# Performance work log

Measured on AMD Instinct MI355X. Metric: run time of the kernel, lower is better.

## Reference

```python
import jax, jax.numpy as jnp
import numpy as np
from jax import lax

THR = 1.0
SLOPE = 25.0
EPS = 1e-5

@jax.custom_vjp
def spike(u):
    # Heaviside with fast-sigmoid surrogate gradient (slope=25)
    return (u > 0.0).astype(u.dtype)

def _spike_fwd(u):
    return (u > 0.0).astype(u.dtype), u

def _spike_bwd(u, g):
    return (g / (SLOPE * jnp.abs(u) + 1.0) ** 2,)

spike.defvjp(_spike_fwd, _spike_bwd)

def lif_scan(inp, beta):
    # inp: (T, B, H); snntorch Leaky, reset_mechanism='subtract', init mem=0
    def step(mem, cur):
        reset = lax.stop_gradient(spike(mem - THR))
        mem = beta * mem + cur - reset * THR
        spk = spike(mem - THR)
        return mem, (spk, mem)
    mem0 = jnp.zeros(inp.shape[1:], inp.dtype)
    _, (spk, mem) = lax.scan(step, mem0, inp)
    return spk, mem

def bn_per_step(h, g, b):
    # h: (T, B, H); training-mode BatchNorm1d applied per timestep over batch
    m = h.mean(axis=1, keepdims=True)
    v = h.var(axis=1, keepdims=True)
    return (h - m) / jnp.sqrt(v + EPS) * g + b

def setup_inputs() -> dict:
    key = jax.random.key(0)
    ks = jax.random.split(key, 16)
    B, T, C = 128, 128, 32
    H, Ts, HOR, K = 512, 4, 96, 3
    s = 0.02
    return {
        "x": jax.random.normal(ks[0], (B, T, C), jnp.float32),
        "conv_w": jax.random.normal(ks[1], (H * Ts, C, K), jnp.float32) * s,
        "conv_b": jnp.zeros((H * Ts,), jnp.float32),
        "bn1_g": jnp.ones((H * Ts,), jnp.float32),
        "bn1_b": jnp.zeros((H * Ts,), jnp.float32),
        "beta_enc": jnp.full((H,), 0.9, jnp.float32),
        "bn2_g": jnp.ones((H,), jnp.float32),
        "bn2_b": jnp.zeros((H,), jnp.float32),
        "beta2": jnp.full((H,), 0.9, jnp.float32),
        "bn3_g": jnp.ones((H,), jnp.float32),
        "bn3_b": jnp.zeros((H,), jnp.float32),
        "beta3": jnp.full((H,), 0.9, jnp.float32),
        "wq": jax.random.normal(ks[2], (H, H), jnp.float32) * s,
        "bq": jnp.zeros((H,), jnp.float32),
        "wk": jax.random.normal(ks[3], (H, H), jnp.float32) * s,
        "bk": jnp.zeros((H,), jnp.float32),
        "wv": jax.random.normal(ks[4], (H, H), jnp.float32) * s,
        "bv": jnp.zeros((H,), jnp.float32),
        "bna_g": jnp.ones((H,), jnp.float32),
        "bna_b": jnp.zeros((H,), jnp.float32),
        "wh": jax.random.normal(ks[5], (HOR, H), jnp.float32) * s,
        "bh": jnp.zeros((HOR,), jnp.float32),
    }

def reference(x, conv_w, conv_b, bn1_g, bn1_b, beta_enc, bn2_g, bn2_b, beta2,
              bn3_g, bn3_b, beta3, wq, bq, wk, bk, wv, bv, bna_g, bna_b, wh, bh):
    B, T, C = x.shape
    H = beta2.shape[0]
    Ts = conv_w.shape[0] // H
    # Conv spike encoder: Conv1d(C -> H*Ts, k, pad=k//2)
    k = conv_w.shape[2]
    h = lax.conv_general_dilated(x.transpose(0, 2, 1), conv_w, (1,), [(k // 2, k // 2)],
                                 dimension_numbers=("NCH", "OIH", "NCH"))
    h = h + conv_b[None, :, None]  # (B, H*Ts, T)
    # BatchNorm1d (training mode): stats over (B, T) per channel, biased var
    m = h.mean((0, 2), keepdims=True)
    v = h.var((0, 2), keepdims=True)
    h = (h - m) / jnp.sqrt(v + EPS) * bn1_g[None, :, None] + bn1_b[None, :, None]
    # (B, H*Ts, T) -> (T*Ts, B, H)
    h = h.transpose(0, 2, 1).reshape(B, T, Ts, H).reshape(B, T * Ts, H).transpose(1, 0, 2)
    spk_enc, _ = lif_scan(h, jnp.clip(beta_enc, 0.0, 0.99))
    # bn2 -> lif2 -> bn3 -> lif3 (BN applied per step in the torch loop)
    h2 = bn_per_step(spk_enc, bn2_g, bn2_b)
    s2, _ = lif_scan(h2, jnp.clip(beta2, 0.0, 0.99))
    h3 = bn_per_step(s2, bn3_g, bn3_b)
    _, mem3 = lif_scan(h3, jnp.clip(beta3, 0.0, 0.99))  # (Ttot, B, H)
    # Spiking attention over membrane trajectory
    xa = mem3.transpose(1, 0, 2)  # (B, Ttot, H)
    Q = xa @ wq.T + bq
    K = xa @ wk.T + bk
    V = xa @ wv.T + bv
    attn = jax.nn.sigmoid(jnp.einsum("btd,bsd->bts", Q, K) * (H ** -0.5))
    feat = jnp.einsum("bts,bsd->btd", attn, V).mean(axis=1)  # (B, H)
    mf = feat.mean(0, keepdims=True)
    vf = feat.var(0, keepdims=True)
    feat = (feat - mf) / jnp.sqrt(vf + EPS) * bna_g + bna_b
    return feat @ wh.T + bh  # (B, horizon)
```

## Files before the change

### kernel.cpp

```cpp
#include <hip/hip_runtime.h>
#include <math.h>

#define EPSF 1e-5f

static constexpr int Bn   = 128;
static constexpr int Tn   = 128;
static constexpr int Cn   = 32;
static constexpr int On   = 2048;
static constexpr int Hn   = 512;
static constexpr int TTn  = 512;
static constexpr int HORn = 96;
static constexpr int BH   = Bn * Hn;
static constexpr float THRf = 1.0f;

__device__ __forceinline__ float bf2f(unsigned short u) {
    union { unsigned int i; float f; } v; v.i = ((unsigned int)u) << 16; return v.f;
}
__device__ __forceinline__ unsigned short f2bf(float f) {
    union { float f; unsigned int i; } v; v.f = f;
    unsigned int r = v.i + 0x7fff + ((v.i >> 16) & 1);
    return (unsigned short)(r >> 16);
}

using bfrag  = __attribute__((ext_vector_type(8))) short;
using f32x4v = __attribute__((ext_vector_type(4))) float;
using us8v   = __attribute__((ext_vector_type(8))) unsigned short;

#define GLD16(gp, lp) __builtin_amdgcn_global_load_lds( \
    (const __attribute__((address_space(1))) void*)(gp), \
    (__attribute__((address_space(3))) void*)(lp), 16, 0, 0)

__global__ __launch_bounds__(256) void im2col_k(const float* __restrict__ x,
    unsigned short* __restrict__ Ph, unsigned short* __restrict__ Pl)
{
    int idx = blockIdx.x * 256 + threadIdx.x;
    int row = idx / 96, kc = idx - row * 96;
    int k = kc >> 5, c = kc & 31;
    int t = row & 127, b = row >> 7;
    int tg = t + k - 1;
    float v = (tg >= 0 && tg < Tn) ? x[((size_t)b * Tn + tg) * Cn + c] : 0.f;
    unsigned short hi = f2bf(v);
    Ph[idx] = hi;
    Pl[idx] = f2bf(v - bf2f(hi));
}

__global__ __launch_bounds__(256) void wprep_k(const float* __restrict__ wconv,
    unsigned short* __restrict__ Wh, unsigned short* __restrict__ Wl)
{
    int idx = blockIdx.x * 256 + threadIdx.x;
    int o = idx / 96, kc = idx - o * 96;
    int k = kc >> 5, c = kc & 31;
    float v = wconv[(size_t)o * 96 + c * 3 + k];
    unsigned short hi = f2bf(v);
    Wh[idx] = hi;
    Wl[idx] = f2bf(v - bf2f(hi));
}

__global__ __launch_bounds__(256) void conv_mfma_k(
    const unsigned short* __restrict__ Ph, const unsigned short* __restrict__ Pl,
    const unsigned short* __restrict__ Wh, const unsigned short* __restrict__ Wl,
    float* __restrict__ raw, float* __restrict__ sums)
{
    const int b  = blockIdx.x;
    const int n0 = blockIdx.y * 128;
    const int tid = threadIdx.x;
    const int lane = tid & 63;
    const int quad = lane >> 4, lr = lane & 15;
    const int wid = tid >> 6, wm = wid & 1, wn = wid >> 1;

    f32x4v acc[4][4] = {};
#pragma unroll
    for (int ks = 0; ks < 3; ks++) {
        const int col = ks * 32 + quad * 8;
        bfrag ah[4], al[4], bh[4], bl[4];
#pragma unroll
        for (int mi = 0; mi < 4; mi++) {
            size_t roff = ((size_t)b * 128 + wm * 64 + mi * 16 + lr) * 96 + col;
            ah[mi] = *(const bfrag*)(Ph + roff);
            al[mi] = *(const bfrag*)(Pl + roff);
        }
#pragma unroll
        for (int ni = 0; ni < 4; ni++) {
            size_t roff = (size_t)(n0 + wn * 64 + ni * 16 + lr) * 96 + col;
            bh[ni] = *(const bfrag*)(Wh + roff);
            bl[ni] = *(const bfrag*)(Wl + roff);
        }
#pragma unroll
        for (int mi = 0; mi < 4; mi++)
#pragma unroll
            for (int ni = 0; ni < 4; ni++) {
                acc[mi][ni] = __builtin_amdgcn_mfma_f32_16x16x32_bf16(
                    ah[mi], bh[ni], acc[mi][ni], 0, 0, 0);
                acc[mi][ni] = __builtin_amdgcn_mfma_f32_16x16x32_bf16(
                    ah[mi], bl[ni], acc[mi][ni], 0, 0, 0);
                acc[mi][ni] = __builtin_amdgcn_mfma_f32_16x16x32_bf16(
                    al[mi], bh[ni], acc[mi][ni], 0, 0, 0);
            }
    }
#pragma unroll
    for (int ni = 0; ni < 4; ni++) {
        int o = n0 + wn * 64 + ni * 16 + lr;
        int ts = o >> 9, hh = o & 511;
        float s = 0.f, ss = 0.f;
#pragma unroll
        for (int mi = 0; mi < 4; mi++)
#pragma unroll
            for (int r = 0; r < 4; r++) {
                int t = wm * 64 + mi * 16 + quad * 4 + r;
                float v = acc[mi][ni][r];
                raw[((size_t)(t * 4 + ts) * Bn + b) * Hn + hh] = v;
                s += v; ss += v * v;
            }
        s  += __shfl_xor(s, 16);  s  += __shfl_xor(s, 32);
        ss += __shfl_xor(ss, 16); ss += __shfl_xor(ss, 32);
        if (quad == 0) {
            atomicAdd(&sums[o], s);
            atomicAdd(&sums[On + o], ss);
        }
    }
}

__global__ void bn1_final_k(const float* __restrict__ sums,
                            const float* __restrict__ g, const float* __restrict__ bb,
                            float* __restrict__ scale, float* __restrict__ shift)
{
    int o = blockIdx.x * 256 + threadIdx.x;
    float m = sums[o] * (1.f / 16384.f);
    float v = sums[On + o] * (1.f / 16384.f) - m * m;
    float sc = g[o] / sqrtf(v + EPSF);
    scale[o] = sc;
    shift[o] = bb[o] - m * sc;
}

__global__ __launch_bounds__(256) void lif1_k(const float* __restrict__ raw,
    const float* __restrict__ scale, const float* __restrict__ shift,
    const float* __restrict__ beta_in, unsigned char* __restrict__ spk)
{
    const int thr = blockIdx.x * 256 + threadIdx.x;
    const int hh = thr & 511;
    const float beta = fminf(fmaxf(beta_in[hh], 0.f), 0.99f);
    float sc[4], sh[4];
#pragma unroll
    for (int ts = 0; ts < 4; ts++) { sc[ts] = scale[ts * Hn + hh]; sh[ts] = shift[ts * Hn + hh]; }
    float mem = 0.f;
    for (int tt = 0; tt < TTn; tt += 8) {
        float cu[8];
#pragma unroll
        for (int u = 0; u < 8; u++) cu[u] = raw[(size_t)(tt + u) * BH + thr];
#pragma unroll
        for (int u = 0; u < 8; u++) {
            float cur = cu[u] * sc[u & 3] + sh[u & 3];
            float reset = mem > THRf ? 1.f : 0.f;
            mem = beta * mem + cur - reset;
            spk[(size_t)(tt + u) * BH + thr] = mem > THRf ? (unsigned char)1 : (unsigned char)0;
        }
    }
}

__global__ __launch_bounds__(256) void bnstep_k(const unsigned char* __restrict__ spk,
    const float* __restrict__ g, const float* __restrict__ bb,
    float* __restrict__ av, float* __restrict__ zv)
{
    const int tt = blockIdx.x;
    const int h0 = threadIdx.x * 2;
    int c0 = 0, c1 = 0;
    const unsigned char* base = spk + (size_t)tt * BH + h0;
#pragma unroll 8
    for (int b = 0; b < Bn; b++) {
        unsigned short v = *(const unsigned short*)(base + (size_t)b * Hn);
        c0 += (v & 0xff); c1 += (v >> 8);
    }
#pragma unroll
    for (int q = 0; q < 2; q++) {
        int hh = h0 + q;
        float p = (q ? c1 : c0) * (1.f / 128.f);
        float inv = 1.f / sqrtf(p - p * p + EPSF);
        float gi = g[hh] * inv;
        float zz = bb[hh] - p * gi;
        av[(size_t)tt * Hn + hh] = gi + zz;
        zv[(size_t)tt * Hn + hh] = zz;
    }
}

__global__ __launch_bounds__(256) void lif2_k(const unsigned char* __restrict__ sin_,
    const float* __restrict__ av, const float* __restrict__ zv,
    const float* __restrict__ beta_in, unsigned char* __restrict__ sout)
{
    const int thr = blockIdx.x * 256 + threadIdx.x;
    const int hh = thr & 511;
    const float beta = fminf(fmaxf(beta_in[hh], 0.f), 0.99f);
    float mem = 0.f;
    for (int tt = 0; tt < TTn; tt += 8) {
        float aa[8], zz[8]; unsigned char ss[8];
#pragma unroll
        for (int u = 0; u < 8; u++) {
            ss[u] = sin_[(size_t)(tt + u) * BH + thr];
            aa[u] = av[(size_t)(tt + u) * Hn + hh];
            zz[u] = zv[(size_t)(tt + u) * Hn + hh];
        }
#pragma unroll
        for (int u = 0; u < 8; u++) {
            float cur = ss[u] ? aa[u] : zz[u];
            float reset = mem > THRf ? 1.f : 0.f;
            mem = beta * mem + cur - reset;
            sout[(size_t)(tt + u) * BH + thr] = mem > THRf ? (unsigned char)1 : (unsigned char)0;
        }
    }
}

__global__ __launch_bounds__(256) void lif3_k(const unsigned char* __restrict__ sin_,
    const float* __restrict__ av, const float* __restrict__ zv,
    const float* __restrict__ beta_in, unsigned short* __restrict__ mem3b)
{
    const int thr = blockIdx.x * 256 + threadIdx.x;
    const int hh = thr & 511;
    const int b = thr >> 9;
    const float beta = fminf(fmaxf(beta_in[hh], 0.f), 0.99f);
    float mem = 0.f;
    for (int tt = 0; tt < TTn; tt += 8) {
        float aa[8], zz[8]; unsigned char ss[8];
#pragma unroll
        for (int u = 0; u < 8; u++) {
            ss[u] = sin_[(size_t)(tt + u) * BH + thr];
            aa[u] = av[(size_t)(tt + u) * Hn + hh];
            zz[u] = zv[(size_t)(tt + u) * Hn + hh];
        }
#pragma unroll
        for (int u = 0; u < 8; u++) {
            float cur = ss[u] ? aa[u] : zz[u];
            float reset = mem > THRf ? 1.f : 0.f;
            mem = beta * mem + cur - reset;
            mem3b[((size_t)b * TTn + (tt + u)) * Hn + hh] = f2bf(mem);
        }
    }
}

__global__ __launch_bounds__(256) void gemm_atb_k(const float* __restrict__ Aw,
    const float* __restrict__ Bw, float* __restrict__ GTp)
{
    __shared__ float As[8][132];
    __shared__ float Bs[8][132];
    const int m0 = blockIdx.x * 128;
    const int n0 = blockIdx.y * 128;
    const int kz = blockIdx.z;
    const int tid = threadIdx.x;
    const int ir = tid >> 5, cl = (tid & 31) * 4;
    const float* Ap = Aw + (size_t)ir * 512 + m0 + cl;
    const float* Bp = Bw + (size_t)ir * 512 + n0 + cl;
    const int tm = tid & 15, tn = tid >> 4;
    float acc[8][8];
#pragma unroll
    for (int i = 0; i < 8; i++)
#pragma unroll
        for (int j = 0; j < 8; j++) acc[i][j] = 0.f;

    for (int i0 = kz * 64; i0 < kz * 64 + 64; i0 += 8) {
        const float4 avv = *(const float4*)(Ap + (size_t)i0 * 512);
        const float4 bvv = *(const float4*)(Bp + (size_t)i0 * 512);
        __syncthreads();
        *(float4*)&As[ir][cl] = avv;
        *(float4*)&Bs[ir][cl] = bvv;
        __syncthreads();
#pragma unroll
        for (int kk = 0; kk < 8; kk++) {
            float4 a0 = *(const float4*)&As[kk][tm * 8];
            float4 a1 = *(const float4*)&As[kk][tm * 8 + 4];
            float4 b0 = *(const float4*)&Bs[kk][tn * 8];
            float4 b1 = *(const float4*)&Bs[kk][tn * 8 + 4];
            float a_[8] = {a0.x, a0.y, a0.z, a0.w, a1.x, a1.y, a1.z, a1.w};
            float b_[8] = {b0.x, b0.y, b0.z, b0.w, b1.x, b1.y, b1.z, b1.w};
#pragma unroll
            for (int i = 0; i < 8; i++)
#pragma unroll
                for (int j = 0; j < 8; j++) acc[i][j] += a_[i] * b_[j];
        }
    }
    float* outp = GTp + (size_t)kz * Hn * Hn;
#pragma unroll
    for (int i = 0; i < 8; i++) {
        size_t rowoff = (size_t)(m0 + tm * 8 + i) * 512 + n0 + tn * 8;
#pragma unroll
        for (int j = 0; j < 8; j++) outp[rowoff + j] = acc[i][j];
    }
}

__global__ void gtred_k(const float* __restrict__ GTp, unsigned short* __restrict__ GT)
{
    int idx = blockIdx.x * 256 + threadIdx.x;
    float s = 0.f;
#pragma unroll
    for (int z = 0; z < 8; z++) s += GTp[(size_t)z * Hn * Hn + idx];
    GT[idx] = f2bf(s);
}

__global__ __launch_bounds__(256) void bias_prep_k(const float* __restrict__ wq,
    const float* __restrict__ wk, const float* __restrict__ bq,
    const float* __restrict__ bk, float* __restrict__ qb, float* __restrict__ kb)
{
    const int blk = blockIdx.x;
    const bool doq = blk < 8;
    const int d0 = (doq ? blk : blk - 8) * 64;
    const float* W    = doq ? wq : wk;
    const float* bvec = doq ? bk : bq;
    const int dl = threadIdx.x & 63, ig = threadIdx.x >> 6;
    float s = 0.f;
    for (int i = ig * 128; i < ig * 128 + 128; i++)
        s += W[(size_t)i * 512 + d0 + dl] * bvec[i];
    __shared__ float red[4][64];
    red[ig][dl] = s;
    __syncthreads();
    if (ig == 0)
        (doq ? qb : kb)[d0 + dl] = red[0][dl] + red[1][dl] + red[2][dl] + red[3][dl];
}

__global__ void c0_k(const float* __restrict__ bq, const float* __restrict__ bk,
                     float* __restrict__ c0)
{
    __shared__ float red[256];
    float p = 0.f;
    for (int i = threadIdx.x; i < 512; i += 256) p += bq[i] * bk[i];
    red[threadIdx.x] = p;
    __syncthreads();
    for (int s = 128; s > 0; s >>= 1) {
        if (threadIdx.x < s) red[threadIdx.x] += red[threadIdx.x + s];
        __syncthreads();
    }
    if (threadIdx.x == 0) c0[0] = red[0];
}

__global__ __launch_bounds__(256) void ygemm_k(const unsigned short* __restrict__ A,
    const unsigned short* __restrict__ GT, const float* __restrict__ qb,
    const float* __restrict__ kb, const float* __restrict__ c0,
    unsigned short* __restrict__ C, float* __restrict__ rowq,
    float* __restrict__ rowk)
{
    __shared__ unsigned short Afull[64 * 512];
    const int m0 = blockIdx.x * 64;
    const int tid = threadIdx.x;
    const int lane = tid & 63;
    const int quad = lane >> 4, lr = lane & 15;
    const int wid = tid >> 6;

#pragma unroll
    for (int i = 0; i < 16; i++) {
        const int r = wid * 16 + i;
        const int cc = lane ^ (i & 7);
        GLD16(A + (size_t)(m0 + r) * 512 + cc * 8, Afull + r * 512);
    }
    __syncthreads();

    const bool dorows = (wid == 0);
    float rq_acc[4] = {0.f, 0.f, 0.f, 0.f};
    float rk_acc[4] = {0.f, 0.f, 0.f, 0.f};

#pragma unroll
    for (int n0t = 0; n0t < 2; n0t++) {
        const int nbase = n0t * 256 + wid * 64;
        const unsigned short* pb[4];
#pragma unroll
        for (int ni = 0; ni < 4; ni++)
            pb[ni] = GT + (size_t)(nbase + ni * 16 + lr) * 512 + quad * 8;
        f32x4v acc[4][4] = {};
        bfrag bcur[4];
#pragma unroll
        for (int ni = 0; ni < 4; ni++) bcur[ni] = *(const bfrag*)pb[ni];
#pragma unroll
        for (int k0 = 0; k0 < 512; k0 += 32) {
            bfrag bnxt[4];
            if (k0 + 32 < 512) {
#pragma unroll
                for (int ni = 0; ni < 4; ni++)
                    bnxt[ni] = *(const bfrag*)(pb[ni] + k0 + 32);
            }
            bfrag af[4];
            const int slot = ((k0 >> 3) + quad) ^ (lr & 7);
#pragma unroll
            for (int mi = 0; mi < 4; mi++)
                af[mi] = *(const bfrag*)&Afull[(mi * 16 + lr) * 512 + slot * 8];
#pragma unroll
            for (int mi = 0; mi < 4; mi++)
#pragma unroll
                for (int ni = 0; ni < 4; ni++)
                    acc[mi][ni] = __builtin_amdgcn_mfma_f32_16x16x32_bf16(
                        af[mi], bcur[ni], acc[mi][ni], 0, 0, 0);
            if (dorows && n0t == 0) {
                const float4 qv0 = *(const float4*)(qb + k0 + quad * 8);
                const float4 qv1 = *(const float4*)(qb + k0 + quad * 8 + 4);
                const float4 kv0 = *(const float4*)(kb + k0 + quad * 8);
                const float4 kv1 = *(const float4*)(kb + k0 + quad * 8 + 4);
                const float qv[8] = {qv0.x, qv0.y, qv0.z, qv0.w, qv1.x, qv1.y, qv1.z, qv1.w};
                const float kv[8] = {kv0.x, kv0.y, kv0.z, kv0.w, kv1.x, kv1.y, kv1.z, kv1.w};
#pragma unroll
                for (int mi = 0; mi < 4; mi++)
#pragma unroll
                    for (int j = 0; j < 8; j++) {
                        float a = bf2f((unsigned short)af[mi][j]);
                        rq_acc[mi] += a * qv[j];
                        rk_acc[mi] += a * kv[j];
                    }
            }
            if (k0 + 32 < 512) {
#pragma unroll
                for (int ni = 0; ni < 4; ni++) bcur[ni] = bnxt[ni];
            }
        }
#pragma unroll
        for (int mi = 0; mi < 4; mi++)
#pragma unroll
            for (int ni = 0; ni < 4; ni++) {
                int col = nbase + ni * 16 + lr;
#pragma unroll
                for (int r = 0; r < 4; r++) {
                    int row = m0 + mi * 16 + quad * 4 + r;
                    C[(size_t)row * 512 + col] = f2bf(acc[mi][ni][r]);
                }
            }
    }
    if (dorows) {
        const float c0v = c0[0];
#pragma unroll
        for (int mi = 0; mi < 4; mi++) {
            float rq = rq_acc[mi], rk = rk_acc[mi];
            rq += __shfl_xor(rq, 16); rq += __shfl_xor(rq, 32);
            rk += __shfl_xor(rk, 16); rk += __shfl_xor(rk, 32);
            if (quad == 0) {
                int row = m0 + mi * 16 + lr;
                rowq[row] = rq + c0v;
                rowk[row] = rk;
            }
        }
    }
}

__global__ __launch_bounds__(256) void scores_k(const unsigned short* __restrict__ Y,
    const unsigned short* __restrict__ Xm, const float* __restrict__ rowq,
    const float* __restrict__ rowk, float* __restrict__ wacc)
{
    __shared__ unsigned short As[128 * 64];
    __shared__ unsigned short Bs[128 * 64];
    __shared__ float colsum[128];
    __shared__ float rq_s[128], rk_s[128];
    const int b  = blockIdx.z;
    const int m0 = blockIdx.x * 128;
    const int n0 = blockIdx.y * 128;
    const int tid = threadIdx.x;
    const int lane = tid & 63;
    const int quad = lane >> 4, lr = lane & 15;
    const int wid = tid >> 6;
    const int wm = wid & 1, wn = wid >> 1;

    if (tid < 128) {
        colsum[tid] = 0.f;
        rq_s[tid] = rowq[(size_t)b * TTn + m0 + tid];
        rk_s[tid] = rowk[(size_t)b * TTn + n0 + tid];
    }

    const int srw = lane >> 3;
    const int scc = (lane & 7) ^ (srw & 7);
    const unsigned short* gA = Y  + (size_t)b * TTn * Hn
        + (size_t)(m0 + wid * 32 + srw) * 512 + scc * 8;
    const unsigned short* gB = Xm + (size_t)b * TTn * Hn
        + (size_t)(n0 + wid * 32 + srw) * 512 + scc * 8;

    f32x4v acc[4][4] = {};
    for (int k0 = 0; k0 < 512; k0 += 64) {
        __syncthreads();
#pragma unroll
        for (int j = 0; j < 4; j++) {
            GLD16(gA + (size_t)j * 8 * 512 + k0, As + (wid * 32 + j * 8) * 64);
            GLD16(gB + (size_t)j * 8 * 512 + k0, Bs + (wid * 32 + j * 8) * 64);
        }
        __syncthreads();
#pragma unroll
        for (int kk = 0; kk < 2; kk++) {
            const int slot = (kk * 4 + quad) ^ (lr & 7);
            bfrag af[4], bf_[4];
#pragma unroll
            for (int mi = 0; mi < 4; mi++)
                af[mi] = *(const bfrag*)&As[(wm * 64 + mi * 16 + lr) * 64 + slot * 8];
#pragma unroll
            for (int ni = 0; ni < 4; ni++)
                bf_[ni] = *(const bfrag*)&Bs[(wn * 64 + ni * 16 + lr) * 64 + slot * 8];
#pragma unroll
            for (int mi = 0; mi < 4; mi++)
#pragma unroll
                for (int ni = 0; ni < 4; ni++)
                    acc[mi][ni] = __builtin_amdgcn_mfma_f32_16x16x32_bf16(
                        af[mi], bf_[ni], acc[mi][ni], 0, 0, 0);
        }
    }
    const float scl = 0.044194173824159216f;
#pragma unroll
    for (int ni = 0; ni < 4; ni++) {
        float s_ln = 0.f;
        float rkv = rk_s[wn * 64 + ni * 16 + lr];
#pragma unroll
        for (int mi = 0; mi < 4; mi++) {
#pragma unroll
            for (int r = 0; r < 4; r++) {
                float rqv = rq_s[wm * 64 + mi * 16 + quad * 4 + r];
                float xv = (acc[mi][ni][r] + rqv + rkv) * scl;
                s_ln += 1.f / (1.f + __expf(-xv));
            }
        }
        atomicAdd(&colsum[wn * 64 + ni * 16 + lr], s_ln);
    }
    __syncthreads();
    if (tid < 128)
        atomicAdd(&wacc[(size_t)b * TTn + n0 + tid], colsum[tid] * (1.f / 512.f));
}

__global__ __launch_bounds__(256) void wsum_k(const float* __restrict__ wacc,
    const unsigned short* __restrict__ mem3b, float* __restrict__ u,
    float* __restrict__ W1)
{
    const int b = blockIdx.x;
    const int tid = threadIdx.x;
    __shared__ float ws_[512];
    __shared__ float red[256];
    ws_[tid] = wacc[(size_t)b * TTn + tid];
    ws_[tid + 256] = wacc[(size_t)b * TTn + tid + 256];
    __syncthreads();
    red[tid] = ws_[tid] + ws_[tid + 256];
    __syncthreads();
    for (int s = 128; s > 0; s >>= 1) {
        if (tid < s) red[tid] += red[tid + s];
        __syncthreads();
    }
    if (tid == 0) W1[b] = red[0];
    float a0 = 0.f, a1 = 0.f;
    const unsigned short* Xb = mem3b + (size_t)b * TTn * Hn;
    for (int s = 0; s < TTn; s++) {
        float w = ws_[s];
        a0 += w * bf2f(Xb[(size_t)s * Hn + tid]);
        a1 += w * bf2f(Xb[(size_t)s * Hn + tid + 256]);
    }
    u[(size_t)b * Hn + tid] = a0;
    u[(size_t)b * Hn + tid + 256] = a1;
}

__global__ __launch_bounds__(256) void feat2_k(const float* __restrict__ u,
    const float* __restrict__ W1, const float* __restrict__ wv,
    const float* __restrict__ bv, float* __restrict__ feat)
{
    const int b = blockIdx.x;
    const int tid = threadIdx.x;
    __shared__ float us[512];
    us[tid] = u[(size_t)b * Hn + tid];
    us[tid + 256] = u[(size_t)b * Hn + tid + 256];
    __syncthreads();
    const float w1 = W1[b];
#pragma unroll
    for (int q = 0; q < 2; q++) {
        int d = tid + q * 256;
        float acc = bv[d] * w1;
        const float* wr = wv + (size_t)d * 512;
        for (int e = 0; e < 512; e += 4) {
            float4 w4 = *(const float4*)(wr + e);
            acc += us[e] * w4.x + us[e+1] * w4.y + us[e+2] * w4.z + us[e+3] * w4.w;
        }
        feat[(size_t)b * Hn + d] = acc;
    }
}

__global__ void bna_k(const float* __restrict__ feat, const float* __restrict__ g,
                      const float* __restrict__ bb, float* __restrict__ featn)
{
    int d = blockIdx.x * 256 + threadIdx.x;
    float s = 0.f, ss = 0.f;
    for (int b = 0; b < Bn; b++) { float v = feat[(size_t)b * Hn + d]; s += v; ss += v * v; }
    float m = s * (1.f / 128.f);
    float var = ss * (1.f / 128.f) - m * m;
    float sc = g[d] / sqrtf(var + EPSF);
    float sh = bb[d] - m * sc;
    for (int b = 0; b < Bn; b++) featn[(size_t)b * Hn + d] = feat[(size_t)b * Hn + d] * sc + sh;
}

__global__ __launch_bounds__(128) void head_k(const float* __restrict__ featn,
    const float* __restrict__ wh, const float* __restrict__ bh, float* __restrict__ out)
{
    const int b = blockIdx.x;
    __shared__ float f[512];
    const int tid = threadIdx.x;
    for (int i = tid; i < 512; i += 128) f[i] = featn[(size_t)b * Hn + i];
    __syncthreads();
    if (tid < HORn) {
        float accv = bh[tid];
        const float* wr = wh + (size_t)tid * Hn;
        for (int d = 0; d < 512; d++) accv += f[d] * wr[d];
        out[(size_t)b * HORn + tid] = accv;
    }
}

__global__ void dbg_k(float* out, float v) { out[0] = v; }

extern "C" void kernel_launch(void* const* d_in, const int* in_sizes, int n_in,
                              void* d_out, int out_size, void* d_ws, size_t ws_size,
                              hipStream_t stream)
{
    (void)in_sizes; (void)n_in;
    const float* x      = (const float*)d_in[0];
    const float* conv_w = (const float*)d_in[1];
    const float* bn1_g  = (const float*)d_in[3];
    const float* bn1_b  = (const float*)d_in[4];
    const float* beta_e = (const float*)d_in[5];
    const float* bn2_g  = (const float*)d_in[6];
    const float* bn2_b  = (const float*)d_in[7];
    const float* beta2  = (const float*)d_in[8];
    const float* bn3_g  = (const float*)d_in[9];
    const float* bn3_b  = (const float*)d_in[10];
    const float* beta3  = (const float*)d_in[11];
    const float* wq     = (const float*)d_in[12];
    const float* bq     = (const float*)d_in[13];
    const float* wk     = (const float*)d_in[14];
    const float* bk     = (const float*)d_in[15];
    const float* wv     = (const float*)d_in[16];
    const float* bv     = (const float*)d_in[17];
    const float* bna_g  = (const float*)d_in[18];
    const float* bna_b  = (const float*)d_in[19];
    const float* wh     = (const float*)d_in[20];
    const float* bh     = (const float*)d_in[21];
    float* out = (float*)d_out;

    char* ws = (char*)d_ws;
    size_t off = 0;
    auto alloc = [&](size_t bytes) {
        char* p = ws + off;
        off += (bytes + 255) & ~(size_t)255;
        return p;
    };
    float* raw          = (float*)alloc((size_t)TTn * BH * 4);
    unsigned char* spk1 = (unsigned char*)alloc((size_t)TTn * BH);
    unsigned char* s2   = (unsigned char*)alloc((size_t)TTn * BH);
    unsigned short* Ph = (unsigned short*)alloc((size_t)Bn * Tn * 96 * 2);
    unsigned short* Pl = (unsigned short*)alloc((size_t)Bn * Tn * 96 * 2);
    unsigned short* Wh = (unsigned short*)alloc((size_t)On * 96 * 2);
    unsigned short* Wl = (unsigned short*)alloc((size_t)On * 96 * 2);
    float* sums   = (float*)alloc(2 * On * 4);
    float* scale1 = (float*)alloc(On * 4);
    float* shift1 = (float*)alloc(On * 4);
    float* a2     = (float*)alloc((size_t)TTn * Hn * 4);
    float* z2     = (float*)alloc((size_t)TTn * Hn * 4);
    float* a3     = (float*)alloc((size_t)TTn * Hn * 4);
    float* z3     = (float*)alloc((size_t)TTn * Hn * 4);
    float* wacc   = (float*)alloc((size_t)Bn * TTn * 4);
    float* GTp    = (float*)alloc((size_t)8 * Hn * Hn * 4);
    unsigned short* GT = (unsigned short*)alloc((size_t)Hn * Hn * 2);
    float* qb     = (float*)alloc(Hn * 4);
    float* kb     = (float*)alloc(Hn * 4);
    float* c0     = (float*)alloc(256);
    float* rowq   = (float*)alloc((size_t)Bn * TTn * 4);
    float* rowk   = (float*)alloc((size_t)Bn * TTn * 4);
    float* u      = (float*)alloc((size_t)Bn * Hn * 4);
    float* W1     = (float*)alloc(Bn * 4);
    float* feat   = (float*)alloc((size_t)Bn * Hn * 4);
    float* featn  = (float*)alloc((size_t)Bn * Hn * 4);
    unsigned short* mem3b = (unsigned short*)raw;
    unsigned short* Y     = (unsigned short*)spk1;

    if (ws_size < off) {
        hipMemsetAsync(d_out, 0, (size_t)out_size * 4, stream);
        dbg_k<<<1, 1, 0, stream>>>(out, (float)ws_size);
        return;
    }

    hipMemsetAsync(sums, 0, 2 * On * 4, stream);
    hipMemsetAsync(wacc, 0, (size_t)Bn * TTn * 4, stream);

    im2col_k<<<(Bn * Tn * 96) / 256, 256, 0, stream>>>(x, Ph, Pl);
    wprep_k<<<(On * 96) / 256, 256, 0, stream>>>(conv_w, Wh, Wl);
    conv_mfma_k<<<dim3(Bn, On / 128), 256, 0, stream>>>(Ph, Pl, Wh, Wl, raw, sums);
    bn1_final_k<<<On / 256, 256, 0, stream>>>(sums, bn1_g, bn1_b, scale1, shift1);
    lif1_k<<<BH / 256, 256, 0, stream>>>(raw, scale1, shift1, beta_e, spk1);
    bnstep_k<<<TTn, 256, 0, stream>>>(spk1, bn2_g, bn2_b, a2, z2);
    lif2_k<<<BH / 256, 256, 0, stream>>>(spk1, a2, z2, beta2, s2);
    bnstep_k<<<TTn, 256, 0, stream>>>(s2, bn3_g, bn3_b, a3, z3);
    lif3_k<<<BH / 256, 256, 0, stream>>>(s2, a3, z3, beta3, mem3b);
    gemm_atb_k<<<dim3(4, 4, 8), 256, 0, stream>>>(wk, wq, GTp);
    gtred_k<<<(Hn * Hn) / 256, 256, 0, stream>>>(GTp, GT);
    bias_prep_k<<<16, 256, 0, stream>>>(wq, wk, bq, bk, qb, kb);
    c0_k<<<1, 256, 0, stream>>>(bq, bk, c0);
    ygemm_k<<<(Bn * TTn) / 64, 256, 0, stream>>>(
        mem3b, GT, qb, kb, c0, Y, rowq, rowk);
    scores_k<<<dim3(TTn / 128, TTn / 128, Bn), 256, 0, stream>>>(Y, mem3b, rowq, rowk, wacc);
    wsum_k<<<Bn, 256, 0, stream>>>(wacc, mem3b, u, W1);
    feat2_k<<<Bn, 256, 0, stream>>>(u, W1, wv, bv, feat);
    bna_k<<<Hn / 256, 256, 0, stream>>>(feat, bna_g, bna_b, featn);
    head_k<<<Bn, 128, 0, stream>>>(featn, wh, bh, out);
}
```

Measured before the change: 550.1 us.

## Retile Y GEMM into 128x128 blocks with LDS-staged A and B K-slices

The Y = mem3·G GEMM kernel now uses a 2D grid of 128x128 output tiles. Both A and B K-slices of 64 are staged through swizzled LDS, and each of the four waves computes a 64x64 sub-tile. Before, each block held a full 64x512 A panel in LDS and streamed B fragments straight from global memory, so every block reread all of G. The new tiling is meant to improve reuse and cut the large LDS footprint, which should raise occupancy. In exchange it adds two barriers per K step with no double buffering, and the row-bias dot products are now done only by the blockIdx.y==0 blocks.

```diff
diff --git a/kernel.cpp b/kernel.cpp
--- a/kernel.cpp
+++ b/kernel.cpp
@@ -329,65 +329,61 @@
 }
 
 __global__ __launch_bounds__(256) void ygemm_k(const unsigned short* __restrict__ A,
-    const unsigned short* __restrict__ GT, const float* __restrict__ qb,
+    const unsigned short* __restrict__ Bsrc, const float* __restrict__ qb,
     const float* __restrict__ kb, const float* __restrict__ c0,
     unsigned short* __restrict__ C, float* __restrict__ rowq,
     float* __restrict__ rowk)
 {
-    __shared__ unsigned short Afull[64 * 512];
-    const int m0 = blockIdx.x * 64;
+    __shared__ unsigned short As[128 * 64];
+    __shared__ unsigned short Bs[128 * 64];
+    const int m0 = blockIdx.x * 128;
+    const int n0 = blockIdx.y * 128;
     const int tid = threadIdx.x;
     const int lane = tid & 63;
     const int quad = lane >> 4, lr = lane & 15;
     const int wid = tid >> 6;
-
-#pragma unroll
-    for (int i = 0; i < 16; i++) {
-        const int r = wid * 16 + i;
-        const int cc = lane ^ (i & 7);
-        GLD16(A + (size_t)(m0 + r) * 512 + cc * 8, Afull + r * 512);
-    }
-    __syncthreads();
-
-    const bool dorows = (wid == 0);
+    const int wm = wid & 1, wn = wid >> 1;
+
+    const int srw = lane >> 3;
+    const int scc = (lane & 7) ^ (srw & 7);
+    const unsigned short* gA = A    + (size_t)(m0 + wid * 32 + srw) * 512 + scc * 8;
+    const unsigned short* gB = Bsrc + (size_t)(n0 + wid * 32 + srw) * 512 + scc * 8;
+
+    const bool dorows = (blockIdx.y == 0) && (wn == 0);
     float rq_acc[4] = {0.f, 0.f, 0.f, 0.f};
     float rk_acc[4] = {0.f, 0.f, 0.f, 0.f};
 
-#pragma unroll
-    for (int n0t = 0; n0t < 2; n0t++) {
-        const int nbase = n0t * 256 + wid * 64;
-        const unsigned short* pb[4];
-#pragma unroll
-        for (int ni = 0; ni < 4; ni++)
-            pb[ni] = GT + (size_t)(nbase + ni * 16 + lr) * 512 + quad * 8;
-        f32x4v acc[4][4] = {};
-        bfrag bcur[4];
-#pragma unroll
-        for (int ni = 0; ni < 4; ni++) bcur[ni] = *(const bfrag*)pb[ni];
-#pragma unroll
-        for (int k0 = 0; k0 < 512; k0 += 32) {
-            bfrag bnxt[4];
-            if (k0 + 32 < 512) {
-#pragma unroll
-                for (int ni = 0; ni < 4; ni++)
-                    bnxt[ni] = *(const bfrag*)(pb[ni] + k0 + 32);
-            }
-            bfrag af[4];
-            const int slot = ((k0 >> 3) + quad) ^ (lr & 7);
+    f32x4v acc[4][4] = {};
+    for (int k0 = 0; k0 < 512; k0 += 64) {
+        __syncthreads();
+#pragma unroll
+        for (int j = 0; j < 4; j++) {
+            GLD16(gA + (size_t)j * 8 * 512 + k0, As + (wid * 32 + j * 8) * 64);
+            GLD16(gB + (size_t)j * 8 * 512 + k0, Bs + (wid * 32 + j * 8) * 64);
+        }
+        __syncthreads();
+#pragma unroll
+        for (int kk = 0; kk < 2; kk++) {
+            const int slot = (kk * 4 + quad) ^ (lr & 7);
+            bfrag af[4], bf_[4];
 #pragma unroll
             for (int mi = 0; mi < 4; mi++)
-                af[mi] = *(const bfrag*)&Afull[(mi * 16 + lr) * 512 + slot * 8];
+                af[mi] = *(const bfrag*)&As[(wm * 64 + mi * 16 + lr) * 64 + slot * 8];
+#pragma unroll
+            for (int ni = 0; ni < 4; ni++)
+                bf_[ni] = *(const bfrag*)&Bs[(wn * 64 + ni * 16 + lr) * 64 + slot * 8];
 #pragma unroll
             for (int mi = 0; mi < 4; mi++)
 #pragma unroll
                 for (int ni = 0; ni < 4; ni++)
                     acc[mi][ni] = __builtin_amdgcn_mfma_f32_16x16x32_bf16(
-                        af[mi], bcur[ni], acc[mi][ni], 0, 0, 0);
-            if (dorows && n0t == 0) {
-                const float4 qv0 = *(const float4*)(qb + k0 + quad * 8);
-                const float4 qv1 = *(const float4*)(qb + k0 + quad * 8 + 4);
-                const float4 kv0 = *(const float4*)(kb + k0 + quad * 8);
-                const float4 kv1 = *(const float4*)(kb + k0 + quad * 8 + 4);
+                        af[mi], bf_[ni], acc[mi][ni], 0, 0, 0);
+            if (dorows) {
+                const int koff = k0 + kk * 32 + quad * 8;
+                const float4 qv0 = *(const float4*)(qb + koff);
+                const float4 qv1 = *(const float4*)(qb + koff + 4);
+                const float4 kv0 = *(const float4*)(kb + koff);
+                const float4 kv1 = *(const float4*)(kb + koff + 4);
                 const float qv[8] = {qv0.x, qv0.y, qv0.z, qv0.w, qv1.x, qv1.y, qv1.z, qv1.w};
                 const float kv[8] = {kv0.x, kv0.y, kv0.z, kv0.w, kv1.x, kv1.y, kv1.z, kv1.w};
 #pragma unroll
@@ -399,23 +395,19 @@
                         rk_acc[mi] += a * kv[j];
                     }
             }
-            if (k0 + 32 < 512) {
-#pragma unroll
-                for (int ni = 0; ni < 4; ni++) bcur[ni] = bnxt[ni];
+        }
+    }
+#pragma unroll
+    for (int mi = 0; mi < 4; mi++)
+#pragma unroll
+        for (int ni = 0; ni < 4; ni++) {
+            int col = n0 + wn * 64 + ni * 16 + lr;
+#pragma unroll
+            for (int r = 0; r < 4; r++) {
+                int row = m0 + wm * 64 + mi * 16 + quad * 4 + r;
+                C[(size_t)row * 512 + col] = f2bf(acc[mi][ni][r]);
             }
         }
-#pragma unroll
-        for (int mi = 0; mi < 4; mi++)
-#pragma unroll
-            for (int ni = 0; ni < 4; ni++) {
-                int col = nbase + ni * 16 + lr;
-#pragma unroll
-                for (int r = 0; r < 4; r++) {
-                    int row = m0 + mi * 16 + quad * 4 + r;
-                    C[(size_t)row * 512 + col] = f2bf(acc[mi][ni][r]);
-                }
-            }
-    }
     if (dorows) {
         const float c0v = c0[0];
 #pragma unroll
@@ -424,7 +416,7 @@
             rq += __shfl_xor(rq, 16); rq += __shfl_xor(rq, 32);
             rk += __shfl_xor(rk, 16); rk += __shfl_xor(rk, 32);
             if (quad == 0) {
-                int row = m0 + mi * 16 + lr;
+                int row = m0 + wm * 64 + mi * 16 + lr;
                 rowq[row] = rq + c0v;
                 rowk[row] = rk;
             }
@@ -680,7 +672,7 @@
     gtred_k<<<(Hn * Hn) / 256, 256, 0, stream>>>(GTp, GT);
     bias_prep_k<<<16, 256, 0, stream>>>(wq, wk, bq, bk, qb, kb);
     c0_k<<<1, 256, 0, stream>>>(bq, bk, c0);
-    ygemm_k<<<(Bn * TTn) / 64, 256, 0, stream>>>(
+    ygemm_k<<<dim3((Bn * TTn) / 128, Hn / 128), 256, 0, stream>>>(
         mem3b, GT, qb, kb, c0, Y, rowq, rowk);
     scores_k<<<dim3(TTn / 128, TTn / 128, Bn), 256, 0, stream>>>(Y, mem3b, rowq, rowk, wacc);
     wsum_k<<<Bn, 256, 0, stream>>>(wacc, mem3b, u, W1);
```

Result: faster. 535.1 us (-2.7%).
